# Kernel tuning notes

Measured on AMD Instinct MI355X. Metric: run time of the kernel, lower is better.

## Reference

```python
import jax, jax.numpy as jnp
import numpy as np

N = 100000
E = 1600000
HEADS = 4
C = 32  # per-head channels; HEADS*C = 128
NEG_SLOPE = 0.2
EPS = 1e-16


def gat_conv(x, src, dst, W, a_src, a_dst, b):
    """One PyG-style GATConv layer (concat=True, self loops already in src/dst).
    x: [N, F_in], W: [F_in, HEADS*C], a_src/a_dst: [HEADS, C], b: [HEADS*C].
    """
    h = (x @ W).reshape(N, HEADS, C)                 # [N, H, C]
    alpha_s = jnp.einsum('nhc,hc->nh', h, a_src)     # [N, H]
    alpha_d = jnp.einsum('nhc,hc->nh', h, a_dst)     # [N, H]
    e = alpha_s[src] + alpha_d[dst]                  # [E, H]
    e = jnp.where(e > 0, e, NEG_SLOPE * e)           # leaky_relu(0.2)
    # segment softmax over incoming edges of each dst node
    m = jax.ops.segment_max(e, dst, num_segments=N)  # [N, H]
    m = jnp.where(jnp.isfinite(m), m, 0.0)
    ex = jnp.exp(e - m[dst])                         # [E, H]
    denom = jax.ops.segment_sum(ex, dst, num_segments=N)
    alpha = ex / (denom[dst] + EPS)                  # [E, H]
    out = jax.ops.segment_sum(alpha[:, :, None] * h[src], dst, num_segments=N)
    return out.reshape(N, HEADS * C) + b


def setup_inputs() -> dict:
    key = jax.random.key(0)
    ks = jax.random.split(key, 6)
    x = jax.random.normal(ks[0], (N, 128), dtype=jnp.float32)
    edge_index = jax.random.randint(ks[1], (2, E), 0, N, dtype=jnp.int64)
    Ws = jax.random.normal(ks[2], (3, 128, 128), dtype=jnp.float32) * 0.1
    att_src = jax.random.normal(ks[3], (3, HEADS, C), dtype=jnp.float32) * 0.1
    att_dst = jax.random.normal(ks[4], (3, HEADS, C), dtype=jnp.float32) * 0.1
    bias = jnp.zeros((3, 128), dtype=jnp.float32)
    return {"x": x, "edge_index": edge_index, "Ws": Ws,
            "att_src": att_src, "att_dst": att_dst, "bias": bias}


def reference(x, edge_index, Ws, att_src, att_dst, bias):
    # PyG GATConv default add_self_loops=True: append i->i edges once.
    loops = jnp.arange(N, dtype=edge_index.dtype)
    src = jnp.concatenate([edge_index[0], loops])
    dst = jnp.concatenate([edge_index[1], loops])
    h = x
    n_layers = Ws.shape[0]
    for l in range(n_layers):
        h = gat_conv(h, src, dst, Ws[l], att_src[l], att_dst[l], bias[l])
        if l < n_layers - 1:
            h = jax.nn.relu(h)  # dropout p given but module run in eval -> identity
    return h
```

## Files before the change

### kernel.cpp

```cpp
#include <hip/hip_runtime.h>

#define HEADS 4
#define CPH 32
#define FDIM 128
#define NEG_SLOPE 0.2f
#define EPS_DEN 1e-16f


__global__ void count_kernel(const int* __restrict__ dst, int* __restrict__ deg, int E) {
    int i = blockIdx.x * blockDim.x + threadIdx.x;
    int stride = gridDim.x * blockDim.x;
    for (; i < E; i += stride) atomicAdd(&deg[dst[i]], 1);
}

__global__ void scan_sum_kernel(const int* __restrict__ deg, int* __restrict__ part, int n) {
    __shared__ int sd[256];
    int t = threadIdx.x;
    int base = blockIdx.x * 1024 + t * 4;
    int s = 0;
#pragma unroll
    for (int j = 0; j < 4; ++j) { int i = base + j; if (i < n) s += deg[i] + 1; }
    sd[t] = s;
    __syncthreads();
    for (int d = 128; d; d >>= 1) { if (t < d) sd[t] += sd[t + d]; __syncthreads(); }
    if (t == 0) part[blockIdx.x] = sd[0];
}

__global__ void scan_part_kernel(int* part, int nblk, int* row_ptr, int n) {
    if (blockIdx.x == 0 && threadIdx.x == 0) {
        int run = 0;
        for (int i = 0; i < nblk; ++i) { int v = part[i]; part[i] = run; run += v; }
        row_ptr[n] = run;
    }
}

__global__ void scan_final_kernel(const int* __restrict__ deg, const int* __restrict__ part,
                                  int* __restrict__ row_ptr, int* __restrict__ cursor, int n) {
    __shared__ int sd[256];
    int t = threadIdx.x;
    int base = blockIdx.x * 1024 + t * 4;
    int v[4]; int s = 0;
#pragma unroll
    for (int j = 0; j < 4; ++j) { int i = base + j; v[j] = (i < n) ? deg[i] + 1 : 0; s += v[j]; }
    sd[t] = s;
    __syncthreads();
    for (int d = 1; d < 256; d <<= 1) {
        int x = sd[t];
        int y = (t >= d) ? sd[t - d] : 0;
        __syncthreads();
        sd[t] = x + y;
        __syncthreads();
    }
    int off = part[blockIdx.x] + sd[t] - s;
#pragma unroll
    for (int j = 0; j < 4; ++j) {
        int i = base + j;
        if (i < n) { row_ptr[i] = off; cursor[i] = off; off += v[j]; }
    }
}

__global__ void fill_kernel(const int* __restrict__ ei, int* __restrict__ cursor,
                            int* __restrict__ csr_src, int E, int N) {
    int ET = E + N;
    int i = blockIdx.x * blockDim.x + threadIdx.x;
    int stride = gridDim.x * blockDim.x;
    for (; i < ET; i += stride) {
        int s, d;
        if (i < E) { s = ei[i]; d = ei[E + i]; }
        else       { s = i - E; d = s; }
        int p = atomicAdd(&cursor[d], 1);
        csr_src[p] = s;
    }
}

#define AS_LD 68

__global__ __launch_bounds__(256) void gemm_alpha_kernel(
        const float* __restrict__ X, const float* __restrict__ W,
        const float* __restrict__ a_src, const float* __restrict__ a_dst,
        float* __restrict__ H, float* __restrict__ ASo, float* __restrict__ ADo, int n) {
    __shared__ float As[32][AS_LD];
    __shared__ float Bs[32][128];
    int tid = threadIdx.x;
    int block_row = blockIdx.x * 64;
    int cg = tid & 15;
    int rg = tid >> 4;
    int r0 = rg * 4;
    int ca = cg * 4;
    int cb = 64 + cg * 4;
    float acc[4][8];
#pragma unroll
    for (int i = 0; i < 4; ++i)
#pragma unroll
        for (int j = 0; j < 8; ++j) acc[i][j] = 0.f;

    for (int k0 = 0; k0 < 128; k0 += 32) {
        for (int t = tid; t < 512; t += 256) {
            int row = t >> 3;
            int kk = (t & 7) << 2;
            int grow = block_row + row;
            float4 v = make_float4(0.f, 0.f, 0.f, 0.f);
            if (grow < n) v = *(const float4*)&X[(size_t)grow * FDIM + k0 + kk];
            As[kk + 0][row] = v.x; As[kk + 1][row] = v.y;
            As[kk + 2][row] = v.z; As[kk + 3][row] = v.w;
        }
        for (int t = tid; t < 1024; t += 256) {
            int kr = t >> 5;
            int c4 = (t & 31) << 2;
            *(float4*)&Bs[kr][c4] = *(const float4*)&W[(size_t)(k0 + kr) * FDIM + c4];
        }
        __syncthreads();
#pragma unroll
        for (int k = 0; k < 32; ++k) {
            float4 a  = *(const float4*)&As[k][r0];
            float4 b1 = *(const float4*)&Bs[k][ca];
            float4 b2 = *(const float4*)&Bs[k][cb];
            float av[4] = {a.x, a.y, a.z, a.w};
            float bv[8] = {b1.x, b1.y, b1.z, b1.w, b2.x, b2.y, b2.z, b2.w};
#pragma unroll
            for (int i = 0; i < 4; ++i)
#pragma unroll
                for (int j = 0; j < 8; ++j) acc[i][j] = fmaf(av[i], bv[j], acc[i][j]);
        }
        __syncthreads();
    }

    int hd_a = cg >> 3;
    int hd_b = 2 + hd_a;
    int co = (cg & 7) * 4;
    float4 wsa = *(const float4*)&a_src[hd_a * CPH + co];
    float4 wsb = *(const float4*)&a_src[hd_b * CPH + co];
    float4 wda = *(const float4*)&a_dst[hd_a * CPH + co];
    float4 wdb = *(const float4*)&a_dst[hd_b * CPH + co];
#pragma unroll
    for (int i = 0; i < 4; ++i) {
        int grow = block_row + r0 + i;
        bool ok = grow < n;
        if (ok) {
            *(float4*)&H[(size_t)grow * FDIM + ca] =
                make_float4(acc[i][0], acc[i][1], acc[i][2], acc[i][3]);
            *(float4*)&H[(size_t)grow * FDIM + cb] =
                make_float4(acc[i][4], acc[i][5], acc[i][6], acc[i][7]);
        }
        float psa = acc[i][0] * wsa.x + acc[i][1] * wsa.y + acc[i][2] * wsa.z + acc[i][3] * wsa.w;
        float psb = acc[i][4] * wsb.x + acc[i][5] * wsb.y + acc[i][6] * wsb.z + acc[i][7] * wsb.w;
        float pda = acc[i][0] * wda.x + acc[i][1] * wda.y + acc[i][2] * wda.z + acc[i][3] * wda.w;
        float pdb = acc[i][4] * wdb.x + acc[i][5] * wdb.y + acc[i][6] * wdb.z + acc[i][7] * wdb.w;
#pragma unroll
        for (int off = 1; off <= 4; off <<= 1) {
            psa += __shfl_xor(psa, off);
            psb += __shfl_xor(psb, off);
            pda += __shfl_xor(pda, off);
            pdb += __shfl_xor(pdb, off);
        }
        if (ok && (cg & 7) == 0) {
            ASo[(size_t)grow * HEADS + hd_a] = psa;
            ASo[(size_t)grow * HEADS + hd_b] = psb;
            ADo[(size_t)grow * HEADS + hd_a] = pda;
            ADo[(size_t)grow * HEADS + hd_b] = pdb;
        }
    }
}

__global__ __launch_bounds__(256) void aggregate_kernel(
        const float* __restrict__ H, const float* __restrict__ ASi, const float* __restrict__ ADi,
        const int* __restrict__ row_ptr, const int* __restrict__ csr_src,
        const float* __restrict__ bias, float* __restrict__ OUT, int n, int relu) {
    int wid = (int)((blockIdx.x * (size_t)blockDim.x + threadIdx.x) >> 6);
    if (wid >= n) return;
    int lane = threadIdx.x & 63;
    int half = lane >> 5;
    int lq   = lane & 31;
    int head = lq >> 3;
    int c0   = lq << 2;

    int start = row_ptr[wid];
    int end   = row_ptr[wid + 1];
    float4 adv = *(const float4*)&ADi[(size_t)wid * HEADS];

    float m = -INFINITY;
    float dn = 0.f;
    float a0 = 0.f, a1 = 0.f, a2 = 0.f, a3 = 0.f;

    for (int base = start; base < end; base += 64) {
        int cnt = min(64, end - base);
        int idx = base + lane;
        float e0 = -INFINITY, e1 = -INFINITY, e2 = -INFINITY, e3 = -INFINITY;
        int my_src = 0;
        if (idx < end) {
            my_src = csr_src[idx];
            float4 as = *(const float4*)&ASi[(size_t)my_src * HEADS];
            float t;
            t = as.x + adv.x; e0 = t > 0.f ? t : NEG_SLOPE * t;
            t = as.y + adv.y; e1 = t > 0.f ? t : NEG_SLOPE * t;
            t = as.z + adv.z; e2 = t > 0.f ? t : NEG_SLOPE * t;
            t = as.w + adv.w; e3 = t > 0.f ? t : NEG_SLOPE * t;
        }
        float q0 = e0, q1 = e1, q2 = e2, q3 = e3;
#pragma unroll
        for (int off = 32; off; off >>= 1) {
            q0 = fmaxf(q0, __shfl_xor(q0, off));
            q1 = fmaxf(q1, __shfl_xor(q1, off));
            q2 = fmaxf(q2, __shfl_xor(q2, off));
            q3 = fmaxf(q3, __shfl_xor(q3, off));
        }
        float cm = head == 0 ? q0 : head == 1 ? q1 : head == 2 ? q2 : q3;
        float nm = fmaxf(m, cm);
        float s = __expf(m - nm);
        a0 *= s; a1 *= s; a2 *= s; a3 *= s; dn *= s;
        m = nm;
        float m0 = __shfl(m, 0), m1 = __shfl(m, 8), m2 = __shfl(m, 16), m3 = __shfl(m, 24);
        float x0 = __expf(e0 - m0);
        float x1 = __expf(e1 - m1);
        float x2 = __expf(e2 - m2);
        float x3 = __expf(e3 - m3);

        int hs = (cnt + 1) >> 1;
        float4 va = make_float4(0.f, 0.f, 0.f, 0.f);
        float4 vb = make_float4(0.f, 0.f, 0.f, 0.f);
        int sA = half;
        if (sA < cnt) {
            int sidx = __shfl(my_src, sA);
            va = *(const float4*)&H[(size_t)sidx * FDIM + c0];
        }
        int sB = half + 2;
        if (sB < cnt) {
            int sidx = __shfl(my_src, sB);
            vb = *(const float4*)&H[(size_t)sidx * FDIM + c0];
        }
        for (int j = 0; j < hs; ++j) {
            int sc = 2 * j + half;
            float t0 = __shfl(x0, sc), t1 = __shfl(x1, sc);
            float t2 = __shfl(x2, sc), t3 = __shfl(x3, sc);
            float xh = head == 0 ? t0 : head == 1 ? t1 : head == 2 ? t2 : t3;
            float4 cv = va;
            va = vb;
            int sn = sc + 4;
            if (sn < cnt) {
                int sidx = __shfl(my_src, sn);
                vb = *(const float4*)&H[(size_t)sidx * FDIM + c0];
            }
            a0 = fmaf(xh, cv.x, a0);
            a1 = fmaf(xh, cv.y, a1);
            a2 = fmaf(xh, cv.z, a2);
            a3 = fmaf(xh, cv.w, a3);
            dn += xh;
        }
    }

    a0 += __shfl_xor(a0, 32);
    a1 += __shfl_xor(a1, 32);
    a2 += __shfl_xor(a2, 32);
    a3 += __shfl_xor(a3, 32);
    dn += __shfl_xor(dn, 32);

    if (half == 0) {
        float inv = 1.f / (dn + EPS_DEN);
        float4 bv = *(const float4*)&bias[c0];
        float o0 = fmaf(a0, inv, bv.x);
        float o1 = fmaf(a1, inv, bv.y);
        float o2 = fmaf(a2, inv, bv.z);
        float o3 = fmaf(a3, inv, bv.w);
        if (relu) {
            o0 = fmaxf(o0, 0.f); o1 = fmaxf(o1, 0.f);
            o2 = fmaxf(o2, 0.f); o3 = fmaxf(o3, 0.f);
        }
        *(float4*)&OUT[(size_t)wid * FDIM + c0] = make_float4(o0, o1, o2, o3);
    }
}


extern "C" void kernel_launch(void* const* d_in, const int* in_sizes, int n_in,
                              void* d_out, int out_size, void* d_ws, size_t ws_size,
                              hipStream_t stream) {
    const int N = in_sizes[0] / FDIM;
    const int E = in_sizes[1] / 2;

    const float* x    = (const float*)d_in[0];
    const int*   ei   = (const int*)d_in[1];
    const float* Ws   = (const float*)d_in[2];
    const float* asrc = (const float*)d_in[3];
    const float* adst = (const float*)d_in[4];
    const float* bias = (const float*)d_in[5];
    float* out = (float*)d_out;

    char* w = (char*)d_ws;
    auto carve = [&](size_t bytes) -> void* {
        void* p = (void*)w;
        w += (bytes + 255) & ~(size_t)255;
        return p;
    };
    float* hA      = (float*)carve((size_t)N * FDIM * 4);
    float* hB      = (float*)carve((size_t)N * FDIM * 4);
    float* ASb     = (float*)carve((size_t)N * HEADS * 4);
    float* ADb     = (float*)carve((size_t)N * HEADS * 4);
    int*   deg     = (int*)carve((size_t)N * 4);
    int*   row_ptr = (int*)carve((size_t)(N + 1) * 4);
    int*   cursor  = (int*)carve((size_t)N * 4);
    int*   csr_src = (int*)carve((size_t)(E + N) * 4);
    int*   part    = (int*)carve(4096);

    hipMemsetAsync(deg, 0, (size_t)N * 4, stream);
    count_kernel<<<2048, 256, 0, stream>>>(ei + E, deg, E);
    int nblk = (N + 1023) / 1024;
    scan_sum_kernel<<<nblk, 256, 0, stream>>>(deg, part, N);
    scan_part_kernel<<<1, 64, 0, stream>>>(part, nblk, row_ptr, N);
    scan_final_kernel<<<nblk, 256, 0, stream>>>(deg, part, row_ptr, cursor, N);
    fill_kernel<<<2048, 256, 0, stream>>>(ei, cursor, csr_src, E, N);

    const float* X = x;
    for (int l = 0; l < 3; ++l) {
        gemm_alpha_kernel<<<(N + 63) / 64, 256, 0, stream>>>(
            X, Ws + (size_t)l * FDIM * FDIM, asrc + l * HEADS * CPH, adst + l * HEADS * CPH,
            hA, ASb, ADb, N);
        float* O = (l == 2) ? out : hB;
        aggregate_kernel<<<(N + 3) / 4, 256, 0, stream>>>(
            hA, ASb, ADb, row_ptr, csr_src, bias + (size_t)l * FDIM, O, N, (l < 2) ? 1 : 0);
        X = hB;
    }
}
```

Measured before the change: 851.5 us.

## Deepen gather prefetch in aggregation and enlarge GEMM tile to 128 rows

The aggregation kernel now keeps six H-row gathers in flight per half-wave instead of two, rotating through six register buffers, so more memory-level parallelism can hide gather latency. The GEMM+alpha kernel moves to a 128x128 block tile with an 8x8 per-thread micro-tile, halving the grid and reusing each W tile across twice as many rows. The alpha head reduction is simplified to a 4-lane shuffle. In exchange, both kernels use more registers, which may lower occupancy, and the GEMM's larger shared-memory tile does the same.

```diff
diff --git a/kernel.cpp b/kernel.cpp
--- a/kernel.cpp
+++ b/kernel.cpp
@@ -73,29 +73,29 @@
     }
 }
 
-#define AS_LD 68
+#define GM_LD 132
 
 __global__ __launch_bounds__(256) void gemm_alpha_kernel(
         const float* __restrict__ X, const float* __restrict__ W,
         const float* __restrict__ a_src, const float* __restrict__ a_dst,
         float* __restrict__ H, float* __restrict__ ASo, float* __restrict__ ADo, int n) {
-    __shared__ float As[32][AS_LD];
+    __shared__ float As[32][GM_LD];
     __shared__ float Bs[32][128];
     int tid = threadIdx.x;
-    int block_row = blockIdx.x * 64;
-    int cg = tid & 15;
-    int rg = tid >> 4;
-    int r0 = rg * 4;
-    int ca = cg * 4;
-    int cb = 64 + cg * 4;
-    float acc[4][8];
-#pragma unroll
-    for (int i = 0; i < 4; ++i)
+    int block_row = blockIdx.x * 128;
+    int tc = tid & 15;
+    int tr = tid >> 4;
+    int r0 = tr * 8;
+    int c0 = tc * 8;
+    float acc[8][8];
+#pragma unroll
+    for (int i = 0; i < 8; ++i)
 #pragma unroll
         for (int j = 0; j < 8; ++j) acc[i][j] = 0.f;
 
     for (int k0 = 0; k0 < 128; k0 += 32) {
-        for (int t = tid; t < 512; t += 256) {
+#pragma unroll
+        for (int t = tid; t < 1024; t += 256) {
             int row = t >> 3;
             int kk = (t & 7) << 2;
             int grow = block_row + row;
@@ -104,6 +104,7 @@
             As[kk + 0][row] = v.x; As[kk + 1][row] = v.y;
             As[kk + 2][row] = v.z; As[kk + 3][row] = v.w;
         }
+#pragma unroll
         for (int t = tid; t < 1024; t += 256) {
             int kr = t >> 5;
             int c4 = (t & 31) << 2;
@@ -112,52 +113,49 @@
         __syncthreads();
 #pragma unroll
         for (int k = 0; k < 32; ++k) {
-            float4 a  = *(const float4*)&As[k][r0];
-            float4 b1 = *(const float4*)&Bs[k][ca];
-            float4 b2 = *(const float4*)&Bs[k][cb];
-            float av[4] = {a.x, a.y, a.z, a.w};
-            float bv[8] = {b1.x, b1.y, b1.z, b1.w, b2.x, b2.y, b2.z, b2.w};
-#pragma unroll
-            for (int i = 0; i < 4; ++i)
+            float4 a0 = *(const float4*)&As[k][r0];
+            float4 a1 = *(const float4*)&As[k][r0 + 4];
+            float4 b0 = *(const float4*)&Bs[k][c0];
+            float4 b1 = *(const float4*)&Bs[k][c0 + 4];
+            float av[8] = {a0.x, a0.y, a0.z, a0.w, a1.x, a1.y, a1.z, a1.w};
+            float bv[8] = {b0.x, b0.y, b0.z, b0.w, b1.x, b1.y, b1.z, b1.w};
+#pragma unroll
+            for (int i = 0; i < 8; ++i)
 #pragma unroll
                 for (int j = 0; j < 8; ++j) acc[i][j] = fmaf(av[i], bv[j], acc[i][j]);
         }
         __syncthreads();
     }
 
-    int hd_a = cg >> 3;
-    int hd_b = 2 + hd_a;
-    int co = (cg & 7) * 4;
-    float4 wsa = *(const float4*)&a_src[hd_a * CPH + co];
-    float4 wsb = *(const float4*)&a_src[hd_b * CPH + co];
-    float4 wda = *(const float4*)&a_dst[hd_a * CPH + co];
-    float4 wdb = *(const float4*)&a_dst[hd_b * CPH + co];
-#pragma unroll
-    for (int i = 0; i < 4; ++i) {
+    int head = tc >> 2;
+    int co = (tc & 3) * 8;
+    float ws[8], wd[8];
+#pragma unroll
+    for (int j = 0; j < 8; ++j) {
+        ws[j] = a_src[head * CPH + co + j];
+        wd[j] = a_dst[head * CPH + co + j];
+    }
+#pragma unroll
+    for (int i = 0; i < 8; ++i) {
         int grow = block_row + r0 + i;
         bool ok = grow < n;
         if (ok) {
-            *(float4*)&H[(size_t)grow * FDIM + ca] =
+            *(float4*)&H[(size_t)grow * FDIM + c0] =
                 make_float4(acc[i][0], acc[i][1], acc[i][2], acc[i][3]);
-            *(float4*)&H[(size_t)grow * FDIM + cb] =
+            *(float4*)&H[(size_t)grow * FDIM + c0 + 4] =
                 make_float4(acc[i][4], acc[i][5], acc[i][6], acc[i][7]);
         }
-        float psa = acc[i][0] * wsa.x + acc[i][1] * wsa.y + acc[i][2] * wsa.z + acc[i][3] * wsa.w;
-        float psb = acc[i][4] * wsb.x + acc[i][5] * wsb.y + acc[i][6] * wsb.z + acc[i][7] * wsb.w;
-        float pda = acc[i][0] * wda.x + acc[i][1] * wda.y + acc[i][2] * wda.z + acc[i][3] * wda.w;
-        float pdb = acc[i][4] * wdb.x + acc[i][5] * wdb.y + acc[i][6] * wdb.z + acc[i][7] * wdb.w;
-#pragma unroll
-        for (int off = 1; off <= 4; off <<= 1) {
-            psa += __shfl_xor(psa, off);
-            psb += __shfl_xor(psb, off);
-            pda += __shfl_xor(pda, off);
-            pdb += __shfl_xor(pdb, off);
-        }
-        if (ok && (cg & 7) == 0) {
-            ASo[(size_t)grow * HEADS + hd_a] = psa;
-            ASo[(size_t)grow * HEADS + hd_b] = psb;
-            ADo[(size_t)grow * HEADS + hd_a] = pda;
-            ADo[(size_t)grow * HEADS + hd_b] = pdb;
+        float ps = 0.f, pd = 0.f;
+#pragma unroll
+        for (int j = 0; j < 8; ++j) {
+            ps = fmaf(acc[i][j], ws[j], ps);
+            pd = fmaf(acc[i][j], wd[j], pd);
+        }
+        ps += __shfl_xor(ps, 1); ps += __shfl_xor(ps, 2);
+        pd += __shfl_xor(pd, 1); pd += __shfl_xor(pd, 2);
+        if (ok && (tc & 3) == 0) {
+            ASo[(size_t)grow * HEADS + head] = ps;
+            ADo[(size_t)grow * HEADS + head] = pd;
         }
     }
 }
@@ -173,6 +171,7 @@
     int lq   = lane & 31;
     int head = lq >> 3;
     int c0   = lq << 2;
+    const float* Hc = H + c0;
 
     int start = row_ptr[wid];
     int end   = row_ptr[wid + 1];
@@ -216,35 +215,43 @@
         float x3 = __expf(e3 - m3);
 
         int hs = (cnt + 1) >> 1;
-        float4 va = make_float4(0.f, 0.f, 0.f, 0.f);
-        float4 vb = make_float4(0.f, 0.f, 0.f, 0.f);
-        int sA = half;
-        if (sA < cnt) {
-            int sidx = __shfl(my_src, sA);
-            va = *(const float4*)&H[(size_t)sidx * FDIM + c0];
-        }
-        int sB = half + 2;
-        if (sB < cnt) {
-            int sidx = __shfl(my_src, sB);
-            vb = *(const float4*)&H[(size_t)sidx * FDIM + c0];
-        }
-        for (int j = 0; j < hs; ++j) {
-            int sc = 2 * j + half;
-            float t0 = __shfl(x0, sc), t1 = __shfl(x1, sc);
-            float t2 = __shfl(x2, sc), t3 = __shfl(x3, sc);
-            float xh = head == 0 ? t0 : head == 1 ? t1 : head == 2 ? t2 : t3;
-            float4 cv = va;
-            va = vb;
-            int sn = sc + 4;
-            if (sn < cnt) {
-                int sidx = __shfl(my_src, sn);
-                vb = *(const float4*)&H[(size_t)sidx * FDIM + c0];
+
+        float4 v0, v1, v2, v3, v4, v5;
+        v0 = v1 = v2 = v3 = v4 = v5 = make_float4(0.f, 0.f, 0.f, 0.f);
+        {
+            int sc;
+            sc = half;      if (sc < cnt) { int si = __shfl(my_src, sc); v0 = *(const float4*)&Hc[(size_t)si * FDIM]; }
+            sc = 2 + half;  if (sc < cnt) { int si = __shfl(my_src, sc); v1 = *(const float4*)&Hc[(size_t)si * FDIM]; }
+            sc = 4 + half;  if (sc < cnt) { int si = __shfl(my_src, sc); v2 = *(const float4*)&Hc[(size_t)si * FDIM]; }
+            sc = 6 + half;  if (sc < cnt) { int si = __shfl(my_src, sc); v3 = *(const float4*)&Hc[(size_t)si * FDIM]; }
+            sc = 8 + half;  if (sc < cnt) { int si = __shfl(my_src, sc); v4 = *(const float4*)&Hc[(size_t)si * FDIM]; }
+            sc = 10 + half; if (sc < cnt) { int si = __shfl(my_src, sc); v5 = *(const float4*)&Hc[(size_t)si * FDIM]; }
+        }
+        auto step = [&](int jj, float4& V) {
+            if (jj < hs) {
+                int sc = 2 * jj + half;
+                float t0 = __shfl(x0, sc), t1 = __shfl(x1, sc);
+                float t2 = __shfl(x2, sc), t3 = __shfl(x3, sc);
+                float xh = head == 0 ? t0 : head == 1 ? t1 : head == 2 ? t2 : t3;
+                a0 = fmaf(xh, V.x, a0);
+                a1 = fmaf(xh, V.y, a1);
+                a2 = fmaf(xh, V.z, a2);
+                a3 = fmaf(xh, V.w, a3);
+                dn += xh;
+                int sn = sc + 12;
+                if (sn < cnt) {
+                    int si = __shfl(my_src, sn);
+                    V = *(const float4*)&Hc[(size_t)si * FDIM];
+                }
             }
-            a0 = fmaf(xh, cv.x, a0);
-            a1 = fmaf(xh, cv.y, a1);
-            a2 = fmaf(xh, cv.z, a2);
-            a3 = fmaf(xh, cv.w, a3);
-            dn += xh;
+        };
+        for (int j0 = 0; j0 < hs; j0 += 6) {
+            step(j0 + 0, v0);
+            step(j0 + 1, v1);
+            step(j0 + 2, v2);
+            step(j0 + 3, v3);
+            step(j0 + 4, v4);
+            step(j0 + 5, v5);
         }
     }
 
@@ -310,7 +317,7 @@
 
     const float* X = x;
     for (int l = 0; l < 3; ++l) {
-        gemm_alpha_kernel<<<(N + 63) / 64, 256, 0, stream>>>(
+        gemm_alpha_kernel<<<(N + 127) / 128, 256, 0, stream>>>(
             X, Ws + (size_t)l * FDIM * FDIM, asrc + l * HEADS * CPH, adst + l * HEADS * CPH,
             hA, ASb, ADb, N);
         float* O = (l == 2) ? out : hB;
```

New measurement: 938.6 us. +10.2%, slower.

## Build CSR via two-pass bucketed scatter instead of global atomic fill

Applied to the files above, without the earlier changes.

Replaces the single-pass CSR fill, which did one global atomicAdd per edge on a per-node cursor and scattered writes randomly, with a two-level bucket sort. Edges are first binned into 512-node buckets using shared-memory histograms and one global atomic per bucket per chunk, and written as (src,dst) pairs into the hB scratch buffer. A second kernel then places each bucket's edges into its CSR slots using shared-memory atomics. The aim is to cut global atomic contention and improve write locality, at the cost of an extra pass over the pair buffer and two more launches.

```diff
diff --git a/kernel.cpp b/kernel.cpp
--- a/kernel.cpp
+++ b/kernel.cpp
@@ -6,6 +6,10 @@
 #define NEG_SLOPE 0.2f
 #define EPS_DEN 1e-16f
 
+#define BSH 9
+#define BKT (1 << BSH)
+#define SCHUNK 4096
+
 
 __global__ void count_kernel(const int* __restrict__ dst, int* __restrict__ deg, int E) {
     int i = blockIdx.x * blockDim.x + threadIdx.x;
@@ -35,7 +39,7 @@
 }
 
 __global__ void scan_final_kernel(const int* __restrict__ deg, const int* __restrict__ part,
-                                  int* __restrict__ row_ptr, int* __restrict__ cursor, int n) {
+                                  int* __restrict__ row_ptr, int n) {
     __shared__ int sd[256];
     int t = threadIdx.x;
     int base = blockIdx.x * 1024 + t * 4;
@@ -55,21 +59,63 @@
 #pragma unroll
     for (int j = 0; j < 4; ++j) {
         int i = base + j;
-        if (i < n) { row_ptr[i] = off; cursor[i] = off; off += v[j]; }
-    }
-}
-
-__global__ void fill_kernel(const int* __restrict__ ei, int* __restrict__ cursor,
-                            int* __restrict__ csr_src, int E, int N) {
+        if (i < n) { row_ptr[i] = off; off += v[j]; }
+    }
+}
+
+__global__ void init_bcur_kernel(const int* __restrict__ row_ptr, int* __restrict__ bcur,
+                                 int N, int NB) {
+    int b = blockIdx.x * blockDim.x + threadIdx.x;
+    if (b < NB) bcur[b] = row_ptr[min(b << BSH, N)];
+}
+
+__global__ __launch_bounds__(256) void bucket_scatter_kernel(
+        const int* __restrict__ ei, int* __restrict__ bcur, int2* __restrict__ pairs,
+        int E, int N, int NB) {
+    __shared__ int hist[512];
+    __shared__ int lcur[512];
     int ET = E + N;
-    int i = blockIdx.x * blockDim.x + threadIdx.x;
-    int stride = gridDim.x * blockDim.x;
-    for (; i < ET; i += stride) {
-        int s, d;
-        if (i < E) { s = ei[i]; d = ei[E + i]; }
-        else       { s = i - E; d = s; }
-        int p = atomicAdd(&cursor[d], 1);
-        csr_src[p] = s;
+    int tid = threadIdx.x;
+    for (int cbase = blockIdx.x * SCHUNK; cbase < ET; cbase += gridDim.x * SCHUNK) {
+        int cend = min(cbase + SCHUNK, ET);
+        for (int b = tid; b < NB; b += 256) hist[b] = 0;
+        __syncthreads();
+        for (int i = cbase + tid; i < cend; i += 256) {
+            int d = (i < E) ? ei[E + i] : (i - E);
+            atomicAdd(&hist[d >> BSH], 1);
+        }
+        __syncthreads();
+        for (int b = tid; b < NB; b += 256) {
+            int c = hist[b];
+            lcur[b] = c ? atomicAdd(&bcur[b], c) : 0;
+        }
+        __syncthreads();
+        for (int i = cbase + tid; i < cend; i += 256) {
+            int s, d;
+            if (i < E) { s = ei[i]; d = ei[E + i]; }
+            else       { s = i - E; d = s; }
+            int p = atomicAdd(&lcur[d >> BSH], 1);
+            pairs[p] = make_int2(s, d);
+        }
+        __syncthreads();
+    }
+}
+
+__global__ __launch_bounds__(256) void csr_from_buckets_kernel(
+        const int2* __restrict__ pairs, const int* __restrict__ row_ptr,
+        int* __restrict__ csr_src, int N) {
+    __shared__ int lcur[BKT];
+    int lo = blockIdx.x << BSH;
+    int hi = min(lo + BKT, N);
+    int tid = threadIdx.x;
+    for (int i = lo + tid; i < hi; i += 256) lcur[i - lo] = row_ptr[i];
+    __syncthreads();
+    int s0 = row_ptr[lo];
+    int s1 = row_ptr[hi];
+    for (int j = s0 + tid; j < s1; j += 256) {
+        int2 pr = pairs[j];
+        int p = atomicAdd(&lcur[pr.y - lo], 1);
+        csr_src[p] = pr.x;
     }
 }
 
@@ -275,6 +321,7 @@
                               hipStream_t stream) {
     const int N = in_sizes[0] / FDIM;
     const int E = in_sizes[1] / 2;
+    const int NB = (N + BKT - 1) >> BSH;
 
     const float* x    = (const float*)d_in[0];
     const int*   ei   = (const int*)d_in[1];
@@ -296,17 +343,21 @@
     float* ADb     = (float*)carve((size_t)N * HEADS * 4);
     int*   deg     = (int*)carve((size_t)N * 4);
     int*   row_ptr = (int*)carve((size_t)(N + 1) * 4);
-    int*   cursor  = (int*)carve((size_t)N * 4);
     int*   csr_src = (int*)carve((size_t)(E + N) * 4);
     int*   part    = (int*)carve(4096);
+    int*   bcur    = (int*)carve(4096);
+    int2*  pairs   = (int2*)hB;
 
     hipMemsetAsync(deg, 0, (size_t)N * 4, stream);
     count_kernel<<<2048, 256, 0, stream>>>(ei + E, deg, E);
     int nblk = (N + 1023) / 1024;
     scan_sum_kernel<<<nblk, 256, 0, stream>>>(deg, part, N);
     scan_part_kernel<<<1, 64, 0, stream>>>(part, nblk, row_ptr, N);
-    scan_final_kernel<<<nblk, 256, 0, stream>>>(deg, part, row_ptr, cursor, N);
-    fill_kernel<<<2048, 256, 0, stream>>>(ei, cursor, csr_src, E, N);
+    scan_final_kernel<<<nblk, 256, 0, stream>>>(deg, part, row_ptr, N);
+    init_bcur_kernel<<<(NB + 255) / 256, 256, 0, stream>>>(row_ptr, bcur, N, NB);
+    int sblk = min(416, (E + N + SCHUNK - 1) / SCHUNK);
+    bucket_scatter_kernel<<<sblk, 256, 0, stream>>>(ei, bcur, pairs, E, N, NB);
+    csr_from_buckets_kernel<<<NB, 256, 0, stream>>>(pairs, row_ptr, csr_src, N);
 
     const float* X = x;
     for (int l = 0; l < 3; ++l) {
```

Result: faster. 797.6 us (-6.3%).
